# Kernel tuning notes

Hardware: AMD Instinct MI355X
Metric: run time of the kernel (lower is better)

## Reference

```python
import jax, jax.numpy as jnp
import numpy as np

NUM_EMBEDDINGS = 1024
EMBEDDING_DIM = 64

def setup_inputs() -> dict:
    key = jax.random.key(0)
    k1, k2 = jax.random.split(key)
    x = jax.random.normal(k1, (16, 64, 64, EMBEDDING_DIM), dtype=jnp.float32)
    # tf.random_uniform_initializer default: U(-0.05, 0.05)
    embeddings = jax.random.uniform(k2, (EMBEDDING_DIM, NUM_EMBEDDINGS),
                                    dtype=jnp.float32, minval=-0.05, maxval=0.05)
    return {"x": x, "embeddings": embeddings}

def reference(x, embeddings):
    input_shape = x.shape
    D = embeddings.shape[0]
    flat = x.reshape(-1, D)  # [N, D]
    # squared L2 distances: ||z||^2 + ||e||^2 - 2 z.e
    similarity = flat @ embeddings  # [N, K]
    distances = (jnp.sum(flat * flat, axis=1, keepdims=True)
                 + jnp.sum(embeddings * embeddings, axis=0)
                 - 2.0 * similarity)
    indices = jnp.argmin(distances, axis=1)  # [N]
    # one-hot @ embeddings.T == gather rows of embeddings.T
    quantized = jnp.take(embeddings.T, indices, axis=0)  # [N, D]
    return quantized.reshape(input_shape)
```

## Files before the change

### kernel.cpp

```cpp
#include <hip/hip_runtime.h>
#include <float.h>

#define K_CODES 1024
#define DIM 64
#define BR 128
#define SAFE_MARGIN_H 1.25e-4f

typedef __attribute__((ext_vector_type(8))) short bf16x8;
typedef __attribute__((ext_vector_type(8))) unsigned short u16x8;
typedef __attribute__((ext_vector_type(4))) float f32x4;

__device__ __forceinline__ unsigned short f2bf(float f) {
    unsigned int u = __float_as_uint(f);
    u += 0x7fff + ((u >> 16) & 1);
    return (unsigned short)(u >> 16);
}
__device__ __forceinline__ float bf2f(unsigned short h) {
    return __uint_as_float(((unsigned int)h) << 16);
}
__device__ __forceinline__ int swz(int row, int byteInRow) {
    return row * 128 + (byteInRow ^ ((row & 7) << 4));
}

__global__ __launch_bounds__(256) void vq_prep2(
    const float* __restrict__ E, float* __restrict__ Et,
    unsigned short* __restrict__ Eh, unsigned short* __restrict__ El,
    float* __restrict__ nrm, float* __restrict__ nrm2, int* __restrict__ cnt)
{
    __shared__ float T[64 * 17];
    const int t = threadIdx.x;
    const int k0 = blockIdx.x * 16;
    if (blockIdx.x == 0 && t == 0) *cnt = 0;
    #pragma unroll
    for (int i = 0; i < 4; ++i) {
        int idx = i * 256 + t;
        int d = idx >> 4, kk = idx & 15;
        T[d * 17 + kk] = E[d * K_CODES + k0 + kk];
    }
    __syncthreads();
    #pragma unroll
    for (int i = 0; i < 4; ++i) {
        int idx = i * 256 + t;
        int kk = idx >> 6, d = idx & 63;
        float v = T[d * 17 + kk];
        Et[(size_t)(k0 + kk) * DIM + d] = v;
        unsigned short h = f2bf(v);
        Eh[(size_t)(k0 + kk) * DIM + d] = h;
        El[(size_t)(k0 + kk) * DIM + d] = f2bf(v - bf2f(h));
    }
    if (t < 16) {
        float s = 0.f;
        #pragma unroll
        for (int d = 0; d < DIM; ++d) {
            float v = T[d * 17 + t];
            s = __builtin_fmaf(v, v, s);
        }
        nrm [k0 + t] = s;
        nrm2[k0 + t] = 0.5f * s;
    }
}

#define LOADG(BH0, BH1, BL0, BL1, NE, g) do {                              \
    int _c = (g) * 16 + col;                                               \
    const unsigned short* _pe = Eh + (size_t)_c * DIM + q * 8;             \
    const unsigned short* _pl = El + (size_t)_c * DIM + q * 8;             \
    BH0 = *(const bf16x8*)(_pe);                                           \
    BH1 = *(const bf16x8*)(_pe + 32);                                      \
    BL0 = *(const bf16x8*)(_pl);                                           \
    BL1 = *(const bf16x8*)(_pl + 32);                                      \
    NE  = nrm2[_c];                                                        \
} while (0)

#define COMP(BH0, BH1, BL0, BL1, NE, g) do {                               \
    int _code = (g) * 16 + col;                                            \
    _Pragma("unroll")                                                      \
    for (int m = 0; m < 2; ++m) {                                          \
        f32x4 acc = {NE, NE, NE, NE};       \
        acc = __builtin_amdgcn_mfma_f32_16x16x32_bf16(aH[m][0], BH0, acc, 0,0,0); \
        acc = __builtin_amdgcn_mfma_f32_16x16x32_bf16(aH[m][1], BH1, acc, 0,0,0); \
        acc = __builtin_amdgcn_mfma_f32_16x16x32_bf16(aH[m][0], BL0, acc, 0,0,0); \
        acc = __builtin_amdgcn_mfma_f32_16x16x32_bf16(aH[m][1], BL1, acc, 0,0,0); \
        acc = __builtin_amdgcn_mfma_f32_16x16x32_bf16(aL[m][0], BH0, acc, 0,0,0); \
        acc = __builtin_amdgcn_mfma_f32_16x16x32_bf16(aL[m][1], BH1, acc, 0,0,0); \
        _Pragma("unroll")                                                  \
        for (int j = 0; j < 4; ++j) {                                      \
            float _d = acc[j];                                             \
            bool _lt = _d < b1[m][j];                                      \
            float _nb1 = fminf(b1[m][j], _d);                              \
            b2[m][j] = __builtin_amdgcn_fmed3f(b1[m][j], b2[m][j], _d);    \
            i1[m][j] = _lt ? _code : i1[m][j];                             \
            b1[m][j] = _nb1;                                               \
        }                                                                  \
    }                                                                      \
} while (0)

__global__ __launch_bounds__(256, 2) void vq_mfma(
    const float* __restrict__ x,
    const unsigned short* __restrict__ Eh,
    const unsigned short* __restrict__ El,
    const float* __restrict__ nrm2,
    const float* __restrict__ Et,
    float* __restrict__ out,
    int* __restrict__ cnt, int* __restrict__ list)
{
    __shared__ char lds[32768 + 512];
    char* Ah = lds;
    char* Al = lds + 16384;
    int*  bidx = (int*)(lds + 32768);

    const int t    = threadIdx.x;
    const int lane = t & 63;
    const int wv   = t >> 6;
    const int col  = lane & 15;
    const int q    = lane >> 4;
    const int koff = q * 16;
    const long r0  = (long)blockIdx.x * BR;

    {
        int row = t >> 1, h = t & 1;
        const float4* src = (const float4*)(x + (r0 + row) * DIM + h * 32);
        float v[32];
        #pragma unroll
        for (int i = 0; i < 8; ++i) {
            float4 f = src[i];
            v[4*i+0] = -f.x; v[4*i+1] = -f.y; v[4*i+2] = -f.z; v[4*i+3] = -f.w;
        }
        unsigned short hi[32], lo[32];
        #pragma unroll
        for (int i = 0; i < 32; ++i) {
            hi[i] = f2bf(v[i]);
            lo[i] = f2bf(v[i] - bf2f(hi[i]));
        }
        #pragma unroll
        for (int s = 0; s < 2; ++s) {
            int seg = h * 2 + s;
            *(u16x8*)(Ah + swz(row, seg*32))      = *(u16x8*)(hi + s*16);
            *(u16x8*)(Ah + swz(row, seg*32 + 16)) = *(u16x8*)(hi + s*16 + 8);
            *(u16x8*)(Al + swz(row, seg*32))      = *(u16x8*)(lo + s*16);
            *(u16x8*)(Al + swz(row, seg*32 + 16)) = *(u16x8*)(lo + s*16 + 8);
        }
    }
    __syncthreads();

    bf16x8 aH[2][2], aL[2][2];
    #pragma unroll
    for (int m = 0; m < 2; ++m) {
        int arow = wv * 32 + m * 16 + col;
        #pragma unroll
        for (int kk = 0; kk < 2; ++kk) {
            aH[m][kk] = *(bf16x8*)(Ah + swz(arow, kk*64 + koff));
            aL[m][kk] = *(bf16x8*)(Al + swz(arow, kk*64 + koff));
        }
    }

    float b1[2][4], b2[2][4];
    int   i1[2][4];
    #pragma unroll
    for (int m = 0; m < 2; ++m)
        #pragma unroll
        for (int j = 0; j < 4; ++j) { b1[m][j] = FLT_MAX; b2[m][j] = FLT_MAX; i1[m][j] = 0x7fffffff; }

    bf16x8 p0h0, p0h1, p0l0, p0l1;  float p0n;
    bf16x8 p1h0, p1h1, p1l0, p1l1;  float p1n;
    bf16x8 p2h0, p2h1, p2l0, p2l1;  float p2n;
    bf16x8 p3h0, p3h1, p3l0, p3l1;  float p3n;
    LOADG(p0h0, p0h1, p0l0, p0l1, p0n, 0);
    LOADG(p1h0, p1h1, p1l0, p1l1, p1n, 1);
    LOADG(p2h0, p2h1, p2l0, p2l1, p2n, 2);
    LOADG(p3h0, p3h1, p3l0, p3l1, p3n, 3);
    #pragma unroll 1
    for (int nt = 0; nt < 64; nt += 4) {
        COMP (p0h0, p0h1, p0l0, p0l1, p0n, nt);
        LOADG(p0h0, p0h1, p0l0, p0l1, p0n, (nt + 4) & 63);
        COMP (p1h0, p1h1, p1l0, p1l1, p1n, nt + 1);
        LOADG(p1h0, p1h1, p1l0, p1l1, p1n, (nt + 5) & 63);
        COMP (p2h0, p2h1, p2l0, p2l1, p2n, nt + 2);
        LOADG(p2h0, p2h1, p2l0, p2l1, p2n, (nt + 6) & 63);
        COMP (p3h0, p3h1, p3l0, p3l1, p3n, nt + 3);
        LOADG(p3h0, p3h1, p3l0, p3l1, p3n, (nt + 7) & 63);
    }

    #pragma unroll
    for (int msk = 1; msk < 16; msk <<= 1) {
        #pragma unroll
        for (int m = 0; m < 2; ++m)
            #pragma unroll
            for (int j = 0; j < 4; ++j) {
                float o1 = __shfl_xor(b1[m][j], msk, 64);
                int   oi = __shfl_xor(i1[m][j], msk, 64);
                float o2 = __shfl_xor(b2[m][j], msk, 64);
                bool take = (o1 < b1[m][j]) || (o1 == b1[m][j] && oi < i1[m][j]);
                float worst = take ? b1[m][j] : o1;
                if (take) { b1[m][j] = o1; i1[m][j] = oi; }
                b2[m][j] = fminf(fminf(b2[m][j], o2), worst);
            }
    }
    if (col == 0) {
        #pragma unroll
        for (int m = 0; m < 2; ++m)
            #pragma unroll
            for (int j = 0; j < 4; ++j) {
                int rowl = wv * 32 + m * 16 + q * 4 + j;
                bidx[rowl] = i1[m][j];
                if (b2[m][j] - b1[m][j] <= SAFE_MARGIN_H) {
                    int p = atomicAdd(cnt, 1);
                    list[p] = (int)(r0 + rowl);
                }
            }
    }
    __syncthreads();

    {
        int rowl = t >> 1, h = t & 1;
        int code = bidx[rowl];
        const float4* src = (const float4*)(Et + (size_t)code * DIM + h * 32);
        float4* dst = (float4*)(out + (size_t)(r0 + rowl) * DIM + h * 32);
        #pragma unroll
        for (int i = 0; i < 8; ++i) dst[i] = src[i];
    }
}

__global__ __launch_bounds__(256) void vq_refine3(
    const float* __restrict__ x, const float* __restrict__ E,
    const float* __restrict__ Et, const float* __restrict__ nrm,
    float* __restrict__ out,
    const int* __restrict__ cnt, const int* __restrict__ list)
{
    __shared__ float zsh[DIM];
    __shared__ float rv[4];
    __shared__ int   ri[4];
    __shared__ int   winner;
    const int n = *cnt;
    const int t = threadIdx.x;
    const int lane = t & 63, wv = t >> 6;

    for (int i = blockIdx.x; i < n; i += gridDim.x) {
        int row = list[i];
        if (t < DIM) zsh[t] = x[(size_t)row * DIM + t];
        __syncthreads();
        float zn = 0.f;
        #pragma unroll
        for (int d = 0; d < DIM; ++d) zn = __builtin_fmaf(zsh[d], zsh[d], zn);
        float a0 = 0.f, a1 = 0.f, a2 = 0.f, a3 = 0.f;
        #pragma unroll
        for (int d = 0; d < DIM; ++d) {
            float zd = zsh[d];
            const float* Ed = E + d * K_CODES;
            a0 = __builtin_fmaf(zd, Ed[t      ], a0);
            a1 = __builtin_fmaf(zd, Ed[t + 256], a1);
            a2 = __builtin_fmaf(zd, Ed[t + 512], a2);
            a3 = __builtin_fmaf(zd, Ed[t + 768], a3);
        }
        float d0 = __builtin_fmaf(-2.f, a0, zn + nrm[t      ]);
        float d1 = __builtin_fmaf(-2.f, a1, zn + nrm[t + 256]);
        float d2 = __builtin_fmaf(-2.f, a2, zn + nrm[t + 512]);
        float d3 = __builtin_fmaf(-2.f, a3, zn + nrm[t + 768]);
        float bv = d0; int bi = t;
        if (d1 < bv) { bv = d1; bi = t + 256; }
        if (d2 < bv) { bv = d2; bi = t + 512; }
        if (d3 < bv) { bv = d3; bi = t + 768; }
        #pragma unroll
        for (int m = 1; m < 64; m <<= 1) {
            float ov = __shfl_xor(bv, m, 64);
            int   oi = __shfl_xor(bi, m, 64);
            if (ov < bv || (ov == bv && oi < bi)) { bv = ov; bi = oi; }
        }
        if (lane == 0) { rv[wv] = bv; ri[wv] = bi; }
        __syncthreads();
        if (t == 0) {
            float v = rv[0]; int b = ri[0];
            #pragma unroll
            for (int w = 1; w < 4; ++w)
                if (rv[w] < v || (rv[w] == v && ri[w] < b)) { v = rv[w]; b = ri[w]; }
            winner = b;
        }
        __syncthreads();
        if (t < DIM) out[(size_t)row * DIM + t] = Et[(size_t)winner * DIM + t];
        __syncthreads();
    }
}

extern "C" void kernel_launch(void* const* d_in, const int* in_sizes, int n_in,
                              void* d_out, int out_size, void* d_ws, size_t ws_size,
                              hipStream_t stream) {
    const float* x = (const float*)d_in[0];
    const float* E = (const float*)d_in[1];
    float* out = (float*)d_out;

    char* ws = (char*)d_ws;
    float*          Et   = (float*)ws;
    unsigned short* Eh   = (unsigned short*)(ws + 262144);
    unsigned short* El   = (unsigned short*)(ws + 393216);
    float*          nrm  = (float*)(ws + 524288);
    float*          nrm2 = (float*)(ws + 528384);
    int*            cnt  = (int*)(ws + 532480);
    int*            list = (int*)(ws + 532736);

    int nrows = in_sizes[0] / DIM;

    vq_prep2<<<64, 256, 0, stream>>>(E, Et, Eh, El, nrm, nrm2, cnt);
    vq_mfma<<<nrows / BR, 256, 0, stream>>>(x, Eh, El, nrm2, Et, out, cnt, list);
    vq_refine3<<<512, 256, 0, stream>>>(x, E, Et, nrm, out, cnt, list);
}
```

Before: 145.8 us.

## Pre-pack codebook bf16 hi/lo in MFMA fragment order for coalesced loads

The prep kernel now writes the bf16 high and low codebook parts in the order each MFMA B fragment is consumed, so every lane in the main kernel loads one contiguous 16-byte chunk at lane*8 and a wave reads a contiguous 1 KB block. Before, each lane read a strided row segment per code. This is meant to cut global and L2 transaction overhead on the codebook stream. The launch bounds minimum-blocks hint also drops from 2 to 1, which lets the compiler use more registers but may lower occupancy.

```diff
diff --git a/kernel.cpp b/kernel.cpp
--- a/kernel.cpp
+++ b/kernel.cpp
@@ -24,7 +24,7 @@
 
 __global__ __launch_bounds__(256) void vq_prep2(
     const float* __restrict__ E, float* __restrict__ Et,
-    unsigned short* __restrict__ Eh, unsigned short* __restrict__ El,
+    unsigned short* __restrict__ Ehp, unsigned short* __restrict__ Elp,
     float* __restrict__ nrm, float* __restrict__ nrm2, int* __restrict__ cnt)
 {
     __shared__ float T[64 * 17];
@@ -42,11 +42,16 @@
     for (int i = 0; i < 4; ++i) {
         int idx = i * 256 + t;
         int kk = idx >> 6, d = idx & 63;
+        int code = k0 + kk;
         float v = T[d * 17 + kk];
-        Et[(size_t)(k0 + kk) * DIM + d] = v;
+        Et[(size_t)code * DIM + d] = v;
         unsigned short h = f2bf(v);
-        Eh[(size_t)(k0 + kk) * DIM + d] = h;
-        El[(size_t)(k0 + kk) * DIM + d] = f2bf(v - bf2f(h));
+        unsigned short l = f2bf(v - bf2f(h));
+        int ct = code >> 4, col = code & 15;
+        int kf = d >> 5, q = (d >> 3) & 3, j = d & 7;
+        size_t pidx = (size_t)(ct * 2 + kf) * 512 + q * 128 + col * 8 + j;
+        Ehp[pidx] = h;
+        Elp[pidx] = l;
     }
     if (t < 16) {
         float s = 0.f;
@@ -61,14 +66,13 @@
 }
 
 #define LOADG(BH0, BH1, BL0, BL1, NE, g) do {                              \
-    int _c = (g) * 16 + col;                                               \
-    const unsigned short* _pe = Eh + (size_t)_c * DIM + q * 8;             \
-    const unsigned short* _pl = El + (size_t)_c * DIM + q * 8;             \
-    BH0 = *(const bf16x8*)(_pe);                                           \
-    BH1 = *(const bf16x8*)(_pe + 32);                                      \
+    const unsigned short* _ph = Ehp + (size_t)(g) * 1024 + lane * 8;       \
+    const unsigned short* _pl = Elp + (size_t)(g) * 1024 + lane * 8;       \
+    BH0 = *(const bf16x8*)(_ph);                                           \
+    BH1 = *(const bf16x8*)(_ph + 512);                                     \
     BL0 = *(const bf16x8*)(_pl);                                           \
-    BL1 = *(const bf16x8*)(_pl + 32);                                      \
-    NE  = nrm2[_c];                                                        \
+    BL1 = *(const bf16x8*)(_pl + 512);                                     \
+    NE  = nrm2[(g) * 16 + col];                                            \
 } while (0)
 
 #define COMP(BH0, BH1, BL0, BL1, NE, g) do {                               \
@@ -94,10 +98,10 @@
     }                                                                      \
 } while (0)
 
-__global__ __launch_bounds__(256, 2) void vq_mfma(
+__global__ __launch_bounds__(256, 1) void vq_mfma(
     const float* __restrict__ x,
-    const unsigned short* __restrict__ Eh,
-    const unsigned short* __restrict__ El,
+    const unsigned short* __restrict__ Ehp,
+    const unsigned short* __restrict__ Elp,
     const float* __restrict__ nrm2,
     const float* __restrict__ Et,
     float* __restrict__ out,
@@ -289,8 +293,8 @@
 
     char* ws = (char*)d_ws;
     float*          Et   = (float*)ws;
-    unsigned short* Eh   = (unsigned short*)(ws + 262144);
-    unsigned short* El   = (unsigned short*)(ws + 393216);
+    unsigned short* Ehp  = (unsigned short*)(ws + 262144);
+    unsigned short* Elp  = (unsigned short*)(ws + 393216);
     float*          nrm  = (float*)(ws + 524288);
     float*          nrm2 = (float*)(ws + 528384);
     int*            cnt  = (int*)(ws + 532480);
@@ -298,7 +302,7 @@
 
     int nrows = in_sizes[0] / DIM;
 
-    vq_prep2<<<64, 256, 0, stream>>>(E, Et, Eh, El, nrm, nrm2, cnt);
-    vq_mfma<<<nrows / BR, 256, 0, stream>>>(x, Eh, El, nrm2, Et, out, cnt, list);
+    vq_prep2<<<64, 256, 0, stream>>>(E, Et, Ehp, Elp, nrm, nrm2, cnt);
+    vq_mfma<<<nrows / BR, 256, 0, stream>>>(x, Ehp, Elp, nrm2, Et, out, cnt, list);
     vq_refine3<<<512, 256, 0, stream>>>(x, E, Et, nrm, out, cnt, list);
 }
```

Measured after the change: 124.4 us. -14.7%, faster.
